# Performance work log

Measured on AMD Instinct MI355X. Metric: run time of the kernel, lower is better.

Reference implementation:

```python
import jax, jax.numpy as jnp
import numpy as np

B, T, C = 8, 2048, 1024
NEG = -1e30  # stand-in for -inf in the stable-softmax running max


def setup_inputs() -> dict:
    key = jax.random.key(0)
    ks = jax.random.split(key, 5)
    x = jax.random.normal(ks[0], (B, T, C), dtype=jnp.float32)
    scales = jnp.arange(C, dtype=jnp.float32) / C  # matches init_weight()
    Wk = jax.random.normal(ks[1], (C, C), dtype=jnp.float32) * 0.02
    Wv = jax.random.normal(ks[2], (C, C), dtype=jnp.float32) * 0.02
    Wr = jax.random.normal(ks[3], (C, C), dtype=jnp.float32) * 0.02
    Wo = jax.random.normal(ks[4], (C, C), dtype=jnp.float32) * 0.02
    return {
        'x': x,
        'w': scales, 'u': scales,
        'mix_k': scales, 'mix_v': scales, 'mix_r': scales,
        'Wk': Wk, 'Wv': Wv, 'Wr': Wr, 'Wo': Wo,
    }


def wkv(w, u, k, v):
    # Numerically-stable RWKV WKV recurrence. k, v: [B, T, C]; w, u: [C]
    w_exp = -jnp.exp(w)  # per-channel log-decay (negative)
    p0 = jnp.zeros(k.shape[::2], k.dtype)      # [B, C] numerator state
    q0 = jnp.zeros(k.shape[::2], k.dtype)      # [B, C] denominator state
    o0 = jnp.full(k.shape[::2], NEG, k.dtype)  # [B, C] running max (log-space)

    def step(carry, kv_t):
        p, q, o = carry
        k_t, v_t = kv_t  # each [B, C]
        uk = u + k_t
        no = jnp.maximum(o, uk)
        A = jnp.exp(o - no)
        Bc = jnp.exp(uk - no)
        out = (A * p + Bc * v_t) / (A * q + Bc)
        wo = w_exp + o
        no2 = jnp.maximum(wo, k_t)
        A2 = jnp.exp(wo - no2)
        B2 = jnp.exp(k_t - no2)
        return (A2 * p + B2 * v_t, A2 * q + B2, no2), out

    kT = jnp.swapaxes(k, 0, 1)  # [T, B, C]
    vT = jnp.swapaxes(v, 0, 1)
    _, outs = jax.lax.scan(step, (p0, q0, o0), (kT, vT))
    return jnp.swapaxes(outs, 0, 1)  # [B, T, C]


def reference(x, w, u, mix_k, mix_v, mix_r, Wk, Wv, Wr, Wo):
    # time_shift: ZeroPad2d((0,0,1,-1)) => shift sequence right by one, zero-pad front
    x_prev = jnp.pad(x, ((0, 0), (1, 0), (0, 0)))[:, :-1]
    # torch.lerp(start=x_prev, end=x, weight=mix)
    xk = x_prev + mix_k * (x - x_prev)
    xv = x_prev + mix_v * (x - x_prev)
    xr = x_prev + mix_r * (x - x_prev)
    k = jnp.einsum('btc,dc->btd', xk, Wk)
    v = jnp.einsum('btc,dc->btd', xv, Wv)
    sr = jax.nn.sigmoid(jnp.einsum('btc,dc->btd', xr, Wr))
    rwkv = sr * wkv(w, u, k, v)
    return jnp.einsum('btc,dc->btd', rwkv, Wo)
```

## Files before the change

### kernel.cpp

```cpp
#include <hip/hip_runtime.h>
#include <hip/hip_bf16.h>
#include <stdint.h>

#define Bb   8
#define Tt   2048
#define Cdim 1024
#define BT   16384
#define SLAB ((size_t)BT * Cdim)

#define NC   32
#define LCH  64
#define CSUB 32

typedef __attribute__((ext_vector_type(4))) float f32x4;
typedef __attribute__((ext_vector_type(8))) short bf16x8;

__device__ inline short f2bs(float f) {
    union { __hip_bfloat16 h; short s; } u;
    u.h = __float2bfloat16(f);
    return u.s;
}
__device__ inline float bs2f(short s) {
    union { short s; __hip_bfloat16 h; } u;
    u.s = s;
    return __bfloat162float(u.h);
}

#define GLOAD_LDS16(g, l) __builtin_amdgcn_global_load_lds( \
    (const __attribute__((address_space(1))) void*)(g),     \
    (__attribute__((address_space(3))) void*)(l), 16, 0, 0)

#define SBAR()      __builtin_amdgcn_s_barrier()

__global__ __launch_bounds__(256) void prep_x(
    const float* __restrict__ x,
    const float* __restrict__ mk,
    const float* __restrict__ mv,
    const float* __restrict__ mr,
    short* __restrict__ xmix)
{
    int idx = blockIdx.x * 256 + threadIdx.x;
    int c8  = idx & (Cdim / 8 - 1);
    int m   = idx >> 7;
    int c0  = c8 << 3;
    int t   = m & (Tt - 1);

    float xs[8], ps[8];
    const float4* xp = (const float4*)(x + (size_t)m * Cdim + c0);
    float4 xa = xp[0], xb = xp[1];
    xs[0]=xa.x; xs[1]=xa.y; xs[2]=xa.z; xs[3]=xa.w;
    xs[4]=xb.x; xs[5]=xb.y; xs[6]=xb.z; xs[7]=xb.w;
    if (t != 0) {
        const float4* pp = (const float4*)(x + (size_t)(m - 1) * Cdim + c0);
        float4 pa = pp[0], pb = pp[1];
        ps[0]=pa.x; ps[1]=pa.y; ps[2]=pa.z; ps[3]=pa.w;
        ps[4]=pb.x; ps[5]=pb.y; ps[6]=pb.z; ps[7]=pb.w;
    } else {
        #pragma unroll
        for (int j = 0; j < 8; ++j) ps[j] = 0.f;
    }

    const float* mixes[3] = {mk, mv, mr};
    #pragma unroll
    for (int z = 0; z < 3; ++z) {
        const float4* mp = (const float4*)(mixes[z] + c0);
        float4 ma = mp[0], mb = mp[1];
        float mm[8];
        mm[0]=ma.x; mm[1]=ma.y; mm[2]=ma.z; mm[3]=ma.w;
        mm[4]=mb.x; mm[5]=mb.y; mm[6]=mb.z; mm[7]=mb.w;
        bf16x8 o;
        #pragma unroll
        for (int j = 0; j < 8; ++j)
            o[j] = f2bs(ps[j] + mm[j] * (xs[j] - ps[j]));
        *(bf16x8*)(xmix + (size_t)z * SLAB + (size_t)m * Cdim + c0) = o;
    }
}

__global__ __launch_bounds__(256) void prep_w(
    const float* __restrict__ Wk, const float* __restrict__ Wv,
    const float* __restrict__ Wr, const float* __restrict__ Wo,
    short* __restrict__ wbf)
{
    int idx = blockIdx.x * 256 + threadIdx.x;
    int z   = idx >> 17;
    int r   = idx & (Cdim * Cdim / 8 - 1);
    const float* src = (z == 0) ? Wk : (z == 1) ? Wv : (z == 2) ? Wr : Wo;
    const float4* sp = (const float4*)(src + (size_t)r * 8);
    float4 a = sp[0], b = sp[1];
    float v[8] = {a.x, a.y, a.z, a.w, b.x, b.y, b.z, b.w};
    bf16x8 o;
    #pragma unroll
    for (int j = 0; j < 8; ++j) o[j] = f2bs(v[j]);
    *(bf16x8*)(wbf + (size_t)z * Cdim * Cdim + (size_t)r * 8) = o;
}

template<int FUSED>
__global__ __launch_bounds__(512, 2) void gemm256(
    const short* __restrict__ Abase,
    const short* __restrict__ Wbase,
    void* __restrict__ o0, void* __restrict__ o1, void* __restrict__ o2)
{
    __shared__ __align__(16) char lds[131072];

    const int tid  = threadIdx.x;
    const int lane = tid & 63;
    const int wv   = tid >> 6;
    const int wm   = wv >> 2, wn = wv & 3;
    const int NT   = Cdim / 64;

    int orig = blockIdx.y * (FUSED ? 12 : 4) + blockIdx.x;
    int xcd  = orig & 7;
    int s    = orig >> 3;
    int z, nt, yt;
    if (FUSED) {
        z  = s >> 5;
        int rem = s & 31;
        nt = rem & 3;
        yt = xcd * 8 + (rem >> 2);
    } else {
        z  = 0;
        nt = s & 3;
        yt = xcd * 8 + (s >> 2);
    }

    const short* A  = Abase + (size_t)z * SLAB;
    const short* Bm = Wbase + (size_t)z * Cdim * Cdim;
    const int m0 = yt * 256;
    const int n0 = nt * 256;

    f32x4 acc[8][4] = {};

    const int lm = lane & 15, lq = lane >> 4, lb7 = lane & 7;
    int ck[2];
    #pragma unroll
    for (int ks = 0; ks < 2; ++ks) ck[ks] = (((ks * 4 + lq) ^ lb7) << 4);
    int aoff[8];
    #pragma unroll
    for (int i = 0; i < 8; ++i) aoff[i] = (i * 16 + lm) * 128;
    int boff[4];
    #pragma unroll
    for (int j = 0; j < 4; ++j) boff[j] = ((wn & 1) * 64 + j * 16 + lm) * 128;
    const int aReg = wm << 14;
    const int bReg = 32768 + ((wn >> 1) << 14);

    const int rlo  = tid >> 3;
    const int clog = (tid & 7) ^ (rlo & 7);
    auto STAGE = [&](int tt, int part) {
        const short* mat = (part < 2) ? A : Bm;
        int rb = ((part < 2) ? m0 : n0) + ((part & 1) << 7);
        const short* g0 = mat + (size_t)(rb + rlo)      * Cdim + (tt << 6) + (clog << 3);
        const short* g1 = mat + (size_t)(rb + 64 + rlo) * Cdim + (tt << 6) + (clog << 3);
        char* l = lds + ((tt & 1) << 16) + (part << 14) + tid * 16;
        GLOAD_LDS16(g0, l);
        GLOAD_LDS16(g1, l + 8192);
    };

    STAGE(0, 0); STAGE(0, 1); STAGE(0, 2); STAGE(0, 3);
    STAGE(1, 0); STAGE(1, 1);
    asm volatile("s_waitcnt vmcnt(4)" ::: "memory");
    SBAR();

    bf16x8 a0[4][2], a4[4][2], b01[2][2], b23[2][2];

    #pragma unroll 1
    for (int kt = 0; kt < NT; ++kt) {
        const char* base = lds + ((kt & 1) << 16);

        #pragma unroll
        for (int i = 0; i < 4; ++i)
            #pragma unroll
            for (int ks = 0; ks < 2; ++ks)
                a0[i][ks] = *(const bf16x8*)(base + aReg + aoff[i] + ck[ks]);
        #pragma unroll
        for (int j = 0; j < 2; ++j)
            #pragma unroll
            for (int ks = 0; ks < 2; ++ks)
                b01[j][ks] = *(const bf16x8*)(base + bReg + boff[j] + ck[ks]);
        #pragma unroll
        for (int i = 0; i < 4; ++i)
            #pragma unroll
            for (int ks = 0; ks < 2; ++ks)
                a4[i][ks] = *(const bf16x8*)(base + aReg + aoff[i + 4] + ck[ks]);
        if (kt + 1 < NT) STAGE(kt + 1, 2);
        __builtin_amdgcn_s_setprio(1);
        #pragma unroll
        for (int ks = 0; ks < 2; ++ks)
            #pragma unroll
            for (int i = 0; i < 4; ++i)
                #pragma unroll
                for (int j = 0; j < 2; ++j)
                    acc[i][j] = __builtin_amdgcn_mfma_f32_16x16x32_bf16(
                        a0[i][ks], b01[j][ks], acc[i][j], 0, 0, 0);
        __builtin_amdgcn_s_setprio(0);
        SBAR();

        #pragma unroll
        for (int j = 0; j < 2; ++j)
            #pragma unroll
            for (int ks = 0; ks < 2; ++ks)
                b23[j][ks] = *(const bf16x8*)(base + bReg + boff[j + 2] + ck[ks]);
        if (kt + 1 < NT) STAGE(kt + 1, 3);
        __builtin_amdgcn_s_setprio(1);
        #pragma unroll
        for (int ks = 0; ks < 2; ++ks)
            #pragma unroll
            for (int i = 0; i < 4; ++i)
                #pragma unroll
                for (int j = 0; j < 2; ++j)
                    acc[i + 4][j] = __builtin_amdgcn_mfma_f32_16x16x32_bf16(
                        a4[i][ks], b01[j][ks], acc[i + 4][j], 0, 0, 0);
        __builtin_amdgcn_s_setprio(0);
        SBAR();

        if (kt + 2 < NT) STAGE(kt + 2, 0);
        __builtin_amdgcn_s_setprio(1);
        #pragma unroll
        for (int ks = 0; ks < 2; ++ks)
            #pragma unroll
            for (int i = 0; i < 4; ++i)
                #pragma unroll
                for (int j = 0; j < 2; ++j)
                    acc[i + 4][j + 2] = __builtin_amdgcn_mfma_f32_16x16x32_bf16(
                        a4[i][ks], b23[j][ks], acc[i + 4][j + 2], 0, 0, 0);
        __builtin_amdgcn_s_setprio(0);
        SBAR();

        if (kt + 2 < NT) STAGE(kt + 2, 1);
        __builtin_amdgcn_s_setprio(1);
        #pragma unroll
        for (int ks = 0; ks < 2; ++ks)
            #pragma unroll
            for (int i = 0; i < 4; ++i)
                #pragma unroll
                for (int j = 0; j < 2; ++j)
                    acc[i][j + 2] = __builtin_amdgcn_mfma_f32_16x16x32_bf16(
                        a0[i][ks], b23[j][ks], acc[i][j + 2], 0, 0, 0);
        __builtin_amdgcn_s_setprio(0);
        if      (kt + 2 < NT) { asm volatile("s_waitcnt vmcnt(4)" ::: "memory"); }
        else if (kt + 1 < NT) { asm volatile("s_waitcnt vmcnt(0)" ::: "memory"); }
        SBAR();
    }

    int col0 = n0 + wn * 64 + lm;
    int row0 = m0 + wm * 128 + (lq << 2);
    short* outb = 0;
    if (FUSED) outb = (short*)((z == 0) ? o0 : (z == 1) ? o1 : o2);
    #pragma unroll
    for (int i = 0; i < 8; ++i) {
        #pragma unroll
        for (int j = 0; j < 4; ++j) {
            #pragma unroll
            for (int r = 0; r < 4; ++r) {
                int row = row0 + i * 16 + r;
                int cc  = col0 + j * 16;
                float vvv = acc[i][j][r];
                if (FUSED) {
                    if (z == 2) vvv = 1.f / (1.f + __expf(-vvv));
                    outb[(size_t)row * Cdim + cc] = f2bs(vvv);
                } else {
                    ((float*)o0)[(size_t)row * Cdim + cc] = vvv;
                }
            }
        }
    }
}

__global__ __launch_bounds__(1024) void wkv_chunked(
    const short* __restrict__ kb, const short* __restrict__ vb,
    const short* __restrict__ srb,
    const float* __restrict__ w, const float* __restrict__ u,
    short* __restrict__ rwkv)
{
    __shared__ float sp[NC][CSUB];
    __shared__ float sq[NC][CSUB];
    __shared__ float so[NC][CSUB];

    int tid = threadIdx.x;
    int cl  = tid & (CSUB - 1);
    int ch  = tid >> 5;
    int b   = blockIdx.x >> 5;
    int cg  = blockIdx.x & 31;
    int c   = cg * CSUB + cl;

    float wexp = -__expf(w[c]);
    float uu   = u[c];
    size_t coff = (size_t)b * Tt * Cdim + (size_t)(ch * LCH) * Cdim + c;

    float p = 0.f, q = 0.f, o = -1e30f;
    #pragma unroll 8
    for (int t = 0; t < LCH; ++t) {
        size_t off = coff + (size_t)t * Cdim;
        float kt = bs2f(kb[off]);
        float vt = bs2f(vb[off]);
        float wo  = wexp + o;
        float no  = fmaxf(wo, kt);
        float A   = __expf(wo - no);
        float B2  = __expf(kt - no);
        p = A * p + B2 * vt;
        q = A * q + B2;
        o = no;
    }
    sp[ch][cl] = p; sq[ch][cl] = q; so[ch][cl] = o;
    __syncthreads();

    if (tid < CSUB) {
        float Ld = wexp * (float)LCH;
        float cp = 0.f, cq = 0.f, co = -1e30f;
        for (int j = 0; j < NC; ++j) {
            float lp = sp[j][tid], lq = sq[j][tid], lo = so[j][tid];
            sp[j][tid] = cp; sq[j][tid] = cq; so[j][tid] = co;
            float od = co + Ld;
            float no = fmaxf(od, lo);
            float A  = __expf(od - no);
            float B2 = __expf(lo - no);
            cp = A * cp + B2 * lp;
            cq = A * cq + B2 * lq;
            co = no;
        }
    }
    __syncthreads();

    p = sp[ch][cl]; q = sq[ch][cl]; o = so[ch][cl];
    #pragma unroll 8
    for (int t = 0; t < LCH; ++t) {
        size_t off = coff + (size_t)t * Cdim;
        float kt = bs2f(kb[off]);
        float vt = bs2f(vb[off]);
        float sr = bs2f(srb[off]);

        float uk  = uu + kt;
        float no  = fmaxf(o, uk);
        float Aa  = __expf(o - no);
        float Bc  = __expf(uk - no);
        float out = (Aa * p + Bc * vt) / (Aa * q + Bc);

        float wo  = wexp + o;
        float no2 = fmaxf(wo, kt);
        float A2  = __expf(wo - no2);
        float B2  = __expf(kt - no2);
        p = A2 * p + B2 * vt;
        q = A2 * q + B2;
        o = no2;

        rwkv[off] = f2bs(sr * out);
    }
}

extern "C" void kernel_launch(void* const* d_in, const int* in_sizes, int n_in,
                              void* d_out, int out_size, void* d_ws, size_t ws_size,
                              hipStream_t stream)
{
    const float* x    = (const float*)d_in[0];
    const float* w    = (const float*)d_in[1];
    const float* u    = (const float*)d_in[2];
    const float* mixk = (const float*)d_in[3];
    const float* mixv = (const float*)d_in[4];
    const float* mixr = (const float*)d_in[5];
    const float* Wk   = (const float*)d_in[6];
    const float* Wv   = (const float*)d_in[7];
    const float* Wr   = (const float*)d_in[8];
    const float* Wo   = (const float*)d_in[9];

    char* ws = (char*)d_ws;
    short* xmix = (short*)ws;
    short* wbf  = (short*)(ws + 3 * SLAB * 2);
    short* rbuf = (short*)(ws + 3 * SLAB * 2 + (size_t)4 * Cdim * Cdim * 2);
    short* rwkv = (short*)ws;
    short* kbuf = (short*)d_out;
    short* vbuf = kbuf + SLAB;

    prep_x<<<BT * Cdim / 8 / 256, 256, 0, stream>>>(x, mixk, mixv, mixr, xmix);
    prep_w<<<4 * Cdim * Cdim / 8 / 256, 256, 0, stream>>>(Wk, Wv, Wr, Wo, wbf);

    dim3 gf(12, BT / 256);
    gemm256<1><<<gf, 512, 0, stream>>>(xmix, wbf, kbuf, vbuf, rbuf);

    wkv_chunked<<<Bb * (Cdim / CSUB), 1024, 0, stream>>>(kbuf, vbuf, rbuf, w, u, rwkv);

    dim3 go(Cdim / 256, BT / 256);
    gemm256<0><<<go, 512, 0, stream>>>(rwkv, wbf + 3 * (size_t)Cdim * Cdim,
                                       (float*)d_out, nullptr, nullptr);
}
```

Before: 240.9 us.

## Split WKV scan into two kernels and merge GEMM barrier phases

The chunked WKV recurrence becomes two launches. The first computes per-chunk summaries and per-quarter totals across 4x more blocks. The second combines the earlier quarters' totals with its own chunk prefix and emits the outputs, which raises parallelism over the single 256-block kernel. It adds global round-trips for the chunk states and an extra launch. Separately, the GEMM main loop drops two of its four barriers per k-step by issuing the B23 loads and paired stages earlier, trading finer-grained overlap and extra register pressure for less synchronisation.

```diff
diff --git a/kernel.cpp b/kernel.cpp
--- a/kernel.cpp
+++ b/kernel.cpp
@@ -8,9 +8,9 @@
 #define BT   16384
 #define SLAB ((size_t)BT * Cdim)
 
-#define NC   32
-#define LCH  64
-#define CSUB 32
+#define NQ    4
+#define NCB   32
+#define LCHQ  16
 
 typedef __attribute__((ext_vector_type(4))) float f32x4;
 typedef __attribute__((ext_vector_type(8))) short bf16x8;
@@ -181,7 +181,12 @@
             #pragma unroll
             for (int ks = 0; ks < 2; ++ks)
                 a4[i][ks] = *(const bf16x8*)(base + aReg + aoff[i + 4] + ck[ks]);
-        if (kt + 1 < NT) STAGE(kt + 1, 2);
+        #pragma unroll
+        for (int j = 0; j < 2; ++j)
+            #pragma unroll
+            for (int ks = 0; ks < 2; ++ks)
+                b23[j][ks] = *(const bf16x8*)(base + bReg + boff[j + 2] + ck[ks]);
+        if (kt + 1 < NT) { STAGE(kt + 1, 2); STAGE(kt + 1, 3); }
         __builtin_amdgcn_s_setprio(1);
         #pragma unroll
         for (int ks = 0; ks < 2; ++ks)
@@ -191,16 +196,6 @@
                 for (int j = 0; j < 2; ++j)
                     acc[i][j] = __builtin_amdgcn_mfma_f32_16x16x32_bf16(
                         a0[i][ks], b01[j][ks], acc[i][j], 0, 0, 0);
-        __builtin_amdgcn_s_setprio(0);
-        SBAR();
-
-        #pragma unroll
-        for (int j = 0; j < 2; ++j)
-            #pragma unroll
-            for (int ks = 0; ks < 2; ++ks)
-                b23[j][ks] = *(const bf16x8*)(base + bReg + boff[j + 2] + ck[ks]);
-        if (kt + 1 < NT) STAGE(kt + 1, 3);
-        __builtin_amdgcn_s_setprio(1);
         #pragma unroll
         for (int ks = 0; ks < 2; ++ks)
             #pragma unroll
@@ -212,7 +207,7 @@
         __builtin_amdgcn_s_setprio(0);
         SBAR();
 
-        if (kt + 2 < NT) STAGE(kt + 2, 0);
+        if (kt + 2 < NT) { STAGE(kt + 2, 0); STAGE(kt + 2, 1); }
         __builtin_amdgcn_s_setprio(1);
         #pragma unroll
         for (int ks = 0; ks < 2; ++ks)
@@ -222,11 +217,6 @@
                 for (int j = 0; j < 2; ++j)
                     acc[i + 4][j + 2] = __builtin_amdgcn_mfma_f32_16x16x32_bf16(
                         a4[i][ks], b23[j][ks], acc[i + 4][j + 2], 0, 0, 0);
-        __builtin_amdgcn_s_setprio(0);
-        SBAR();
-
-        if (kt + 2 < NT) STAGE(kt + 2, 1);
-        __builtin_amdgcn_s_setprio(1);
         #pragma unroll
         for (int ks = 0; ks < 2; ++ks)
             #pragma unroll
@@ -265,37 +255,37 @@
     }
 }
 
-__global__ __launch_bounds__(1024) void wkv_chunked(
+__global__ __launch_bounds__(1024) void wkv_sum(
     const short* __restrict__ kb, const short* __restrict__ vb,
-    const short* __restrict__ srb,
-    const float* __restrict__ w, const float* __restrict__ u,
-    short* __restrict__ rwkv)
-{
-    __shared__ float sp[NC][CSUB];
-    __shared__ float sq[NC][CSUB];
-    __shared__ float so[NC][CSUB];
+    const float* __restrict__ w,
+    float* __restrict__ spg, float* __restrict__ sqg, float* __restrict__ sog,
+    float* __restrict__ qtp, float* __restrict__ qtq, float* __restrict__ qto)
+{
+    __shared__ float sp[NCB][32], sq[NCB][32], so[NCB][32];
 
     int tid = threadIdx.x;
-    int cl  = tid & (CSUB - 1);
+    int cl  = tid & 31;
     int ch  = tid >> 5;
-    int b   = blockIdx.x >> 5;
-    int cg  = blockIdx.x & 31;
-    int c   = cg * CSUB + cl;
+    int bx  = blockIdx.x;
+    int b   = bx >> 7;
+    int rest = bx & 127;
+    int qi  = rest >> 5;
+    int cg  = rest & 31;
+    int c   = cg * 32 + cl;
 
     float wexp = -__expf(w[c]);
-    float uu   = u[c];
-    size_t coff = (size_t)b * Tt * Cdim + (size_t)(ch * LCH) * Cdim + c;
+    size_t coff = (size_t)b * Tt * Cdim + (size_t)(qi * (NCB * LCHQ) + ch * LCHQ) * Cdim + c;
 
     float p = 0.f, q = 0.f, o = -1e30f;
-    #pragma unroll 8
-    for (int t = 0; t < LCH; ++t) {
+    #pragma unroll
+    for (int t = 0; t < LCHQ; ++t) {
         size_t off = coff + (size_t)t * Cdim;
         float kt = bs2f(kb[off]);
         float vt = bs2f(vb[off]);
-        float wo  = wexp + o;
-        float no  = fmaxf(wo, kt);
-        float A   = __expf(wo - no);
-        float B2  = __expf(kt - no);
+        float wo = wexp + o;
+        float no = fmaxf(wo, kt);
+        float A  = __expf(wo - no);
+        float B2 = __expf(kt - no);
         p = A * p + B2 * vt;
         q = A * q + B2;
         o = no;
@@ -303,26 +293,81 @@
     sp[ch][cl] = p; sq[ch][cl] = q; so[ch][cl] = o;
     __syncthreads();
 
-    if (tid < CSUB) {
-        float Ld = wexp * (float)LCH;
+    if (tid < 32) {
+        float Ld = wexp * (float)LCHQ;
         float cp = 0.f, cq = 0.f, co = -1e30f;
-        for (int j = 0; j < NC; ++j) {
-            float lp = sp[j][tid], lq = sq[j][tid], lo = so[j][tid];
+        for (int j = 0; j < NCB; ++j) {
+            float lp = sp[j][tid], lq_ = sq[j][tid], lo = so[j][tid];
             sp[j][tid] = cp; sq[j][tid] = cq; so[j][tid] = co;
             float od = co + Ld;
             float no = fmaxf(od, lo);
             float A  = __expf(od - no);
             float B2 = __expf(lo - no);
             cp = A * cp + B2 * lp;
-            cq = A * cq + B2 * lq;
+            cq = A * cq + B2 * lq_;
             co = no;
         }
+        int cc = cg * 32 + tid;
+        size_t qidx = ((size_t)b * NQ + qi) * Cdim + cc;
+        qtp[qidx] = cp; qtq[qidx] = cq; qto[qidx] = co;
     }
     __syncthreads();
 
-    p = sp[ch][cl]; q = sq[ch][cl]; o = so[ch][cl];
-    #pragma unroll 8
-    for (int t = 0; t < LCH; ++t) {
+    size_t gidx = ((size_t)b * (NQ * NCB) + qi * NCB + ch) * Cdim + c;
+    spg[gidx] = sp[ch][cl]; sqg[gidx] = sq[ch][cl]; sog[gidx] = so[ch][cl];
+}
+
+__global__ __launch_bounds__(1024) void wkv_emit(
+    const short* __restrict__ kb, const short* __restrict__ vb,
+    const short* __restrict__ srb,
+    const float* __restrict__ w, const float* __restrict__ u,
+    const float* __restrict__ spg, const float* __restrict__ sqg,
+    const float* __restrict__ sog,
+    const float* __restrict__ qtp, const float* __restrict__ qtq,
+    const float* __restrict__ qto,
+    short* __restrict__ rwkv)
+{
+    int tid = threadIdx.x;
+    int cl  = tid & 31;
+    int ch  = tid >> 5;
+    int bx  = blockIdx.x;
+    int b   = bx >> 7;
+    int rest = bx & 127;
+    int qi  = rest >> 5;
+    int cg  = rest & 31;
+    int c   = cg * 32 + cl;
+
+    float wexp = -__expf(w[c]);
+    float uu   = u[c];
+
+    float fp = 0.f, fq = 0.f, fo = -1e30f;
+    for (int j = 0; j < qi; ++j) {
+        size_t qidx = ((size_t)b * NQ + j) * Cdim + c;
+        float lp = qtp[qidx], lq_ = qtq[qidx], lo = qto[qidx];
+        float od = fo + wexp * (float)(NCB * LCHQ);
+        float no = fmaxf(od, lo);
+        float A  = __expf(od - no);
+        float B2 = __expf(lo - no);
+        fp = A * fp + B2 * lp;
+        fq = A * fq + B2 * lq_;
+        fo = no;
+    }
+    {
+        size_t gidx = ((size_t)b * (NQ * NCB) + qi * NCB + ch) * Cdim + c;
+        float lp = spg[gidx], lq_ = sqg[gidx], lo = sog[gidx];
+        float od = fo + wexp * (float)(LCHQ * ch);
+        float no = fmaxf(od, lo);
+        float A  = __expf(od - no);
+        float B2 = __expf(lo - no);
+        fp = A * fp + B2 * lp;
+        fq = A * fq + B2 * lq_;
+        fo = no;
+    }
+
+    float p = fp, q = fq, o = fo;
+    size_t coff = (size_t)b * Tt * Cdim + (size_t)(qi * (NCB * LCHQ) + ch * LCHQ) * Cdim + c;
+    #pragma unroll
+    for (int t = 0; t < LCHQ; ++t) {
         size_t off = coff + (size_t)t * Cdim;
         float kt = bs2f(kb[off]);
         float vt = bs2f(vb[off]);
@@ -369,13 +414,26 @@
     short* kbuf = (short*)d_out;
     short* vbuf = kbuf + SLAB;
 
+    float* fbase = (float*)(ws + SLAB * 2);
+    const size_t NST = (size_t)Bb * (NQ * NCB) * Cdim;
+    const size_t NQT = (size_t)Bb * NQ * Cdim;
+    float* spg = fbase;
+    float* sqg = fbase + NST;
+    float* sog = fbase + 2 * NST;
+    float* qtp = fbase + 3 * NST;
+    float* qtq = fbase + 3 * NST + NQT;
+    float* qto = fbase + 3 * NST + 2 * NQT;
+
     prep_x<<<BT * Cdim / 8 / 256, 256, 0, stream>>>(x, mixk, mixv, mixr, xmix);
     prep_w<<<4 * Cdim * Cdim / 8 / 256, 256, 0, stream>>>(Wk, Wv, Wr, Wo, wbf);
 
     dim3 gf(12, BT / 256);
     gemm256<1><<<gf, 512, 0, stream>>>(xmix, wbf, kbuf, vbuf, rbuf);
 
-    wkv_chunked<<<Bb * (Cdim / CSUB), 1024, 0, stream>>>(kbuf, vbuf, rbuf, w, u, rwkv);
+    wkv_sum<<<Bb * NQ * (Cdim / 32), 1024, 0, stream>>>(
+        kbuf, vbuf, w, spg, sqg, sog, qtp, qtq, qto);
+    wkv_emit<<<Bb * NQ * (Cdim / 32), 1024, 0, stream>>>(
+        kbuf, vbuf, rbuf, w, u, spg, sqg, sog, qtp, qtq, qto, rwkv);
 
     dim3 go(Cdim / 256, BT / 256);
     gemm256<0><<<go, 512, 0, stream>>>(rwkv, wbf + 3 * (size_t)Cdim * Cdim,
```

Result: slower. 250.1 us (+3.8%).
